# Optimization experiments

Hardware: AMD Instinct MI355X
Metric: run time of the kernel (lower is better)

## Reference

```python
import jax, jax.numpy as jnp
import numpy as np

BN_EPS = 1e-5

def setup_inputs() -> dict:
    key = jax.random.key(0)
    ks = jax.random.split(key, 7)
    B, D, A = 16384, 768, 51
    s = 1.0 / np.sqrt(D)
    return {
        "x": jax.random.normal(ks[0], (B, D), dtype=jnp.float32),
        "W_embed": jax.random.uniform(ks[1], (D, D), minval=-s, maxval=s, dtype=jnp.float32),
        "b_embed": jax.random.uniform(ks[2], (D,), minval=-s, maxval=s, dtype=jnp.float32),
        "W_attr": jax.random.uniform(ks[3], (A, D), minval=-s, maxval=s, dtype=jnp.float32),  # stacked per-attribute (dim->1) heads
        "b_attr": jax.random.uniform(ks[4], (A,), minval=-s, maxval=s, dtype=jnp.float32),
        "gamma": jnp.ones((A,), dtype=jnp.float32),
        "beta": jnp.zeros((A,), dtype=jnp.float32),
    }

def reference(x, W_embed, b_embed, W_attr, b_attr, gamma, beta):
    # word_embed: Linear(dim, dim)
    h = x @ W_embed.T + b_embed                      # [B, D]
    # fused per-attribute heads: cat of attr_num (dim->1) linears == one (dim->attr_num) matmul
    logits = h @ W_attr.T + b_attr                    # [B, A]
    # BatchNorm1d (training mode: batch statistics, biased variance)
    mean = jnp.mean(logits, axis=0)
    var = jnp.var(logits, axis=0)
    y = (logits - mean) * jax.lax.rsqrt(var + BN_EPS) * gamma + beta
    return y
```

## Files before the change

kernel.cpp:

```cpp
#include <hip/hip_runtime.h>
#include <hip/hip_bf16.h>

typedef _Float16 halfx8 __attribute__((ext_vector_type(8)));
typedef _Float16 halfx4 __attribute__((ext_vector_type(4)));
typedef float floatx4 __attribute__((ext_vector_type(4)));

#define GLOBAL_AS __attribute__((address_space(1)))
#define LDS_AS __attribute__((address_space(3)))

__device__ __forceinline__ void async_copy_16(const _Float16* g, _Float16* l) {
    __builtin_amdgcn_global_load_lds((GLOBAL_AS void*)g, (LDS_AS void*)l, 16, 0, 0);
}

#define PM 16384
#define PD 768
#define PA 51
#define PA_PAD 64


__global__ void convert_w_kernel(const float* __restrict__ We, const float* __restrict__ Wa,
                                 _Float16* __restrict__ we16, _Float16* __restrict__ wa16,
                                 float* __restrict__ stats) {
    int b = blockIdx.x, t = threadIdx.x;
    if (b < 576) {
        int idx = b * 256 + t;
        float4 v = ((const float4*)We)[idx];
        halfx4 h;
        h[0] = (_Float16)v.x; h[1] = (_Float16)v.y; h[2] = (_Float16)v.z; h[3] = (_Float16)v.w;
        *(halfx4*)(we16 + (size_t)idx * 4) = h;
    } else if (b < 624) {
        int j = (b - 576) * 256 + t;
        halfx4 h;
        if (j < (PA * PD) / 4) {
            float4 v = ((const float4*)Wa)[j];
            h[0] = (_Float16)v.x; h[1] = (_Float16)v.y; h[2] = (_Float16)v.z; h[3] = (_Float16)v.w;
        } else {
            h[0] = (_Float16)0.f; h[1] = (_Float16)0.f; h[2] = (_Float16)0.f; h[3] = (_Float16)0.f;
        }
        *(halfx4*)(wa16 + (size_t)j * 4) = h;
    } else {
        if (t < 128) stats[t] = 0.f;
    }
}

__global__ __launch_bounds__(256, 3) void gemm1_kernel(
    const float* __restrict__ X,
    const _Float16* __restrict__ B,
    const float* __restrict__ bias,
    _Float16* __restrict__ H)
{
    __shared__ _Float16 As[128 * 64];
    __shared__ _Float16 Bs[128 * 64];
    const int tid = threadIdx.x;
    const int wave = tid >> 6;
    const int lane = tid & 63;
    const int quad = lane >> 4;
    const int l16 = lane & 15;
    const int wm = wave >> 1;
    const int wn = wave & 1;

    int b = blockIdx.x;
    int xcd = b & 7;
    int q = b >> 3;
    int mt = xcd * 16 + (q & 15);
    int nt = q >> 4;
    const int row0 = mt * 128;
    const int col0 = nt * 128;

    const int r_in = lane >> 3;
    const int csw = (lane & 7) ^ r_in;
    const int ksw = csw * 8;

    const float* Ag = X + (size_t)row0 * PD + ksw;
    const _Float16* Bg = B + (size_t)col0 * PD + ksw;

    floatx4 acc[4][4];
    #pragma unroll
    for (int i = 0; i < 4; ++i)
        #pragma unroll
        for (int j = 0; j < 4; ++j)
            acc[i][j] = (floatx4){0.f, 0.f, 0.f, 0.f};

    for (int kt = 0; kt < PD; kt += 64) {
        #pragma unroll
        for (int j = 0; j < 4; ++j) {
            int i = wave * 4 + j;
            const float* ap = Ag + (size_t)(i * 8 + r_in) * PD + kt;
            float4 v0 = *(const float4*)(ap);
            float4 v1 = *(const float4*)(ap + 4);
            halfx8 h;
            h[0] = (_Float16)v0.x; h[1] = (_Float16)v0.y;
            h[2] = (_Float16)v0.z; h[3] = (_Float16)v0.w;
            h[4] = (_Float16)v1.x; h[5] = (_Float16)v1.y;
            h[6] = (_Float16)v1.z; h[7] = (_Float16)v1.w;
            *(halfx8*)&As[(i * 8 + r_in) * 64 + (lane & 7) * 8] = h;
            async_copy_16(Bg + (size_t)(i * 8 + r_in) * PD + kt, &Bs[i * 512]);
        }
        __syncthreads();
        #pragma unroll
        for (int ks = 0; ks < 2; ++ks) {
            halfx8 af[4], bf[4];
            #pragma unroll
            for (int mi = 0; mi < 4; ++mi)
                af[mi] = *(const halfx8*)&As[(wm * 64 + mi * 16 + l16) * 64 +
                                             (((ks * 4 + quad) ^ (l16 & 7)) << 3)];
            #pragma unroll
            for (int ni = 0; ni < 4; ++ni)
                bf[ni] = *(const halfx8*)&Bs[(wn * 64 + ni * 16 + l16) * 64 +
                                             (((ks * 4 + quad) ^ (l16 & 7)) << 3)];
            #pragma unroll
            for (int mi = 0; mi < 4; ++mi)
                #pragma unroll
                for (int ni = 0; ni < 4; ++ni)
                    acc[mi][ni] = __builtin_amdgcn_mfma_f32_16x16x32_f16(af[mi], bf[ni], acc[mi][ni], 0, 0, 0);
        }
        __syncthreads();
    }

    #pragma unroll
    for (int ni = 0; ni < 4; ++ni) {
        int col = col0 + wn * 64 + ni * 16 + l16;
        float bv = bias[col];
        #pragma unroll
        for (int mi = 0; mi < 4; ++mi) {
            int rowb = row0 + wm * 64 + mi * 16 + quad * 4;
            #pragma unroll
            for (int r = 0; r < 4; ++r)
                H[(size_t)(rowb + r) * PD + col] = (_Float16)(acc[mi][ni][r] + bv);
        }
    }
}

__global__ __launch_bounds__(256) void gemm2_kernel(
    const _Float16* __restrict__ Hm,
    const _Float16* __restrict__ Wa,
    const float* __restrict__ b_attr,
    float* __restrict__ logits,
    float* __restrict__ stats)
{
    __shared__ _Float16 As[64 * 64];
    __shared__ _Float16 Bs[64 * 64];
    __shared__ float s_sum[64];
    __shared__ float s_ssq[64];
    const int tid = threadIdx.x;
    const int wave = tid >> 6;
    const int lane = tid & 63;
    const int quad = lane >> 4;
    const int l16 = lane & 15;
    const int row0 = blockIdx.x * 64;
    const int r_in = lane >> 3;
    const int ksw = ((lane & 7) ^ r_in) * 8;

    if (tid < 64) { s_sum[tid] = 0.f; s_ssq[tid] = 0.f; }

    const _Float16* Ag = Hm + (size_t)row0 * PD + ksw;
    const _Float16* Bg = Wa + ksw;

    floatx4 acc[4];
    #pragma unroll
    for (int j = 0; j < 4; ++j)
        acc[j] = (floatx4){0.f, 0.f, 0.f, 0.f};

    for (int kt = 0; kt < PD; kt += 64) {
        #pragma unroll
        for (int j = 0; j < 2; ++j) {
            int i = wave * 2 + j;
            async_copy_16(Ag + (size_t)(i * 8 + r_in) * PD + kt, &As[i * 512]);
            async_copy_16(Bg + (size_t)(i * 8 + r_in) * PD + kt, &Bs[i * 512]);
        }
        __syncthreads();
        #pragma unroll
        for (int ks = 0; ks < 2; ++ks) {
            halfx8 af, bf[4];
            af = *(const halfx8*)&As[(wave * 16 + l16) * 64 +
                                     (((ks * 4 + quad) ^ (l16 & 7)) << 3)];
            #pragma unroll
            for (int ni = 0; ni < 4; ++ni)
                bf[ni] = *(const halfx8*)&Bs[(ni * 16 + l16) * 64 +
                                             (((ks * 4 + quad) ^ (l16 & 7)) << 3)];
            #pragma unroll
            for (int ni = 0; ni < 4; ++ni)
                acc[ni] = __builtin_amdgcn_mfma_f32_16x16x32_f16(af, bf[ni], acc[ni], 0, 0, 0);
        }
        __syncthreads();
    }

    #pragma unroll
    for (int ni = 0; ni < 4; ++ni) {
        int col = ni * 16 + l16;
        if (col < PA) {
            float bv = b_attr[col];
            float ps = 0.f, pss = 0.f;
            int rowb = row0 + wave * 16 + quad * 4;
            #pragma unroll
            for (int r = 0; r < 4; ++r) {
                float v = acc[ni][r] + bv;
                logits[(size_t)(rowb + r) * PA + col] = v;
                ps += v; pss += v * v;
            }
            atomicAdd(&s_sum[col], ps);
            atomicAdd(&s_ssq[col], pss);
        }
    }
    __syncthreads();
    if (tid < PA) {
        atomicAdd(&stats[tid], s_sum[tid]);
        atomicAdd(&stats[64 + tid], s_ssq[tid]);
    }
}

__global__ void bn_finalize_kernel(const float* __restrict__ logits,
                                   const float* __restrict__ stats,
                                   const float* __restrict__ gamma,
                                   const float* __restrict__ beta,
                                   float* __restrict__ out, int total) {
    __shared__ float s_scale[PA];
    __shared__ float s_shift[PA];
    int t = threadIdx.x;
    if (t < PA) {
        const float invB = 1.0f / (float)PM;
        float mean = stats[t] * invB;
        float var = stats[64 + t] * invB - mean * mean;
        float inv = rsqrtf(var + 1e-5f);
        float g = gamma[t] * inv;
        s_scale[t] = g;
        s_shift[t] = beta[t] - mean * g;
    }
    __syncthreads();
    int idx = blockIdx.x * 256 + t;
    if (idx < total) {
        int col = idx % PA;
        out[idx] = logits[idx] * s_scale[col] + s_shift[col];
    }
}

extern "C" void kernel_launch(void* const* d_in, const int* in_sizes, int n_in,
                              void* d_out, int out_size, void* d_ws, size_t ws_size,
                              hipStream_t stream) {
    const float* x       = (const float*)d_in[0];
    const float* W_embed = (const float*)d_in[1];
    const float* b_embed = (const float*)d_in[2];
    const float* W_attr  = (const float*)d_in[3];
    const float* b_attr  = (const float*)d_in[4];
    const float* gamma   = (const float*)d_in[5];
    const float* beta    = (const float*)d_in[6];
    float* out = (float*)d_out;

    char* ws = (char*)d_ws;
    _Float16* we16   = (_Float16*)(ws);
    _Float16* wa16   = (_Float16*)(ws + 1179648);
    _Float16* h_f16  = (_Float16*)(ws + 1277952);
    float*    logits = (float*)   (ws + 26443776);
    float*    stats  = (float*)   (ws + 29786112);

    convert_w_kernel<<<625, 256, 0, stream>>>(W_embed, W_attr, we16, wa16, stats);
    gemm1_kernel<<<768, 256, 0, stream>>>(x, we16, b_embed, h_f16);
    gemm2_kernel<<<256, 256, 0, stream>>>(h_f16, wa16, b_attr, logits, stats);
    bn_finalize_kernel<<<3264, 256, 0, stream>>>(logits, stats, gamma, beta, out, PM * PA);
}
```

Measured before the change: 155.2 us.

## Fold the two linear layers into one combined weight before the skinny GEMM

Precomputes Wc = W_attr·W_embed (51x768) and a combined bias in a small kernel, so the large 16384x768x768 GEMM and the fp16 H intermediate go away. The remaining kernel streams x directly into LDS as fp32 with async copies and converts it to fp16 at fragment load, then multiplies by the folded weight. This removes most of the FLOPs and the H round-trip through memory. In exchange it adds a serial precompute of about 30M FMAs on 53 blocks and changes rounding order, since Wc is formed in fp32 and then cast to fp16.

```diff
diff --git a/kernel.cpp b/kernel.cpp
--- a/kernel.cpp
+++ b/kernel.cpp
@@ -8,172 +8,114 @@
 #define GLOBAL_AS __attribute__((address_space(1)))
 #define LDS_AS __attribute__((address_space(3)))
 
-__device__ __forceinline__ void async_copy_16(const _Float16* g, _Float16* l) {
+__device__ __forceinline__ void async_copy_16(const void* g, void* l) {
     __builtin_amdgcn_global_load_lds((GLOBAL_AS void*)g, (LDS_AS void*)l, 16, 0, 0);
 }
 
 #define PM 16384
 #define PD 768
 #define PA 51
-#define PA_PAD 64
-
-
-__global__ void convert_w_kernel(const float* __restrict__ We, const float* __restrict__ Wa,
-                                 _Float16* __restrict__ we16, _Float16* __restrict__ wa16,
-                                 float* __restrict__ stats) {
+
+
+__global__ __launch_bounds__(192) void precompute_kernel(
+    const float* __restrict__ We, const float* __restrict__ Wa,
+    const float* __restrict__ b_embed, const float* __restrict__ b_attr,
+    _Float16* __restrict__ wc16, float* __restrict__ bc, float* __restrict__ stats)
+{
     int b = blockIdx.x, t = threadIdx.x;
-    if (b < 576) {
-        int idx = b * 256 + t;
-        float4 v = ((const float4*)We)[idx];
+    if (b < PA) {
+        int d0 = t * 4;
+        const float* war = Wa + (size_t)b * PD;
+        float a0 = 0.f, a1 = 0.f, a2 = 0.f, a3 = 0.f;
+        #pragma unroll 8
+        for (int k = 0; k < PD; ++k) {
+            float w = war[k];
+            floatx4 v = *(const floatx4*)(We + (size_t)k * PD + d0);
+            a0 += w * v[0]; a1 += w * v[1]; a2 += w * v[2]; a3 += w * v[3];
+        }
         halfx4 h;
-        h[0] = (_Float16)v.x; h[1] = (_Float16)v.y; h[2] = (_Float16)v.z; h[3] = (_Float16)v.w;
-        *(halfx4*)(we16 + (size_t)idx * 4) = h;
-    } else if (b < 624) {
-        int j = (b - 576) * 256 + t;
-        halfx4 h;
-        if (j < (PA * PD) / 4) {
-            float4 v = ((const float4*)Wa)[j];
-            h[0] = (_Float16)v.x; h[1] = (_Float16)v.y; h[2] = (_Float16)v.z; h[3] = (_Float16)v.w;
-        } else {
-            h[0] = (_Float16)0.f; h[1] = (_Float16)0.f; h[2] = (_Float16)0.f; h[3] = (_Float16)0.f;
-        }
-        *(halfx4*)(wa16 + (size_t)j * 4) = h;
+        h[0] = (_Float16)a0; h[1] = (_Float16)a1; h[2] = (_Float16)a2; h[3] = (_Float16)a3;
+        *(halfx4*)(wc16 + (size_t)b * PD + d0) = h;
+    } else if (b == PA) {
+        halfx8 z;
+        #pragma unroll
+        for (int j = 0; j < 8; ++j) z[j] = (_Float16)0.f;
+        for (int i = t; i < 1248; i += 192)
+            *(halfx8*)(wc16 + PA * PD + i * 8) = z;
+        if (t < 128) stats[t] = 0.f;
     } else {
-        if (t < 128) stats[t] = 0.f;
-    }
-}
-
-__global__ __launch_bounds__(256, 3) void gemm1_kernel(
+        if (t < PA) {
+            const float* war = Wa + (size_t)t * PD;
+            float acc = 0.f;
+            #pragma unroll 4
+            for (int k = 0; k < PD; k += 4) {
+                floatx4 w = *(const floatx4*)(war + k);
+                floatx4 e = *(const floatx4*)(b_embed + k);
+                acc += w[0] * e[0] + w[1] * e[1] + w[2] * e[2] + w[3] * e[3];
+            }
+            bc[t] = acc + b_attr[t];
+        }
+    }
+}
+
+__global__ __launch_bounds__(256) void skinny_gemm_kernel(
     const float* __restrict__ X,
-    const _Float16* __restrict__ B,
-    const float* __restrict__ bias,
-    _Float16* __restrict__ H)
-{
-    __shared__ _Float16 As[128 * 64];
-    __shared__ _Float16 Bs[128 * 64];
-    const int tid = threadIdx.x;
-    const int wave = tid >> 6;
-    const int lane = tid & 63;
-    const int quad = lane >> 4;
-    const int l16 = lane & 15;
-    const int wm = wave >> 1;
-    const int wn = wave & 1;
-
-    int b = blockIdx.x;
-    int xcd = b & 7;
-    int q = b >> 3;
-    int mt = xcd * 16 + (q & 15);
-    int nt = q >> 4;
-    const int row0 = mt * 128;
-    const int col0 = nt * 128;
-
-    const int r_in = lane >> 3;
-    const int csw = (lane & 7) ^ r_in;
-    const int ksw = csw * 8;
-
-    const float* Ag = X + (size_t)row0 * PD + ksw;
-    const _Float16* Bg = B + (size_t)col0 * PD + ksw;
-
-    floatx4 acc[4][4];
-    #pragma unroll
-    for (int i = 0; i < 4; ++i)
-        #pragma unroll
-        for (int j = 0; j < 4; ++j)
-            acc[i][j] = (floatx4){0.f, 0.f, 0.f, 0.f};
-
-    for (int kt = 0; kt < PD; kt += 64) {
-        #pragma unroll
-        for (int j = 0; j < 4; ++j) {
-            int i = wave * 4 + j;
-            const float* ap = Ag + (size_t)(i * 8 + r_in) * PD + kt;
-            float4 v0 = *(const float4*)(ap);
-            float4 v1 = *(const float4*)(ap + 4);
-            halfx8 h;
-            h[0] = (_Float16)v0.x; h[1] = (_Float16)v0.y;
-            h[2] = (_Float16)v0.z; h[3] = (_Float16)v0.w;
-            h[4] = (_Float16)v1.x; h[5] = (_Float16)v1.y;
-            h[6] = (_Float16)v1.z; h[7] = (_Float16)v1.w;
-            *(halfx8*)&As[(i * 8 + r_in) * 64 + (lane & 7) * 8] = h;
-            async_copy_16(Bg + (size_t)(i * 8 + r_in) * PD + kt, &Bs[i * 512]);
-        }
-        __syncthreads();
-        #pragma unroll
-        for (int ks = 0; ks < 2; ++ks) {
-            halfx8 af[4], bf[4];
-            #pragma unroll
-            for (int mi = 0; mi < 4; ++mi)
-                af[mi] = *(const halfx8*)&As[(wm * 64 + mi * 16 + l16) * 64 +
-                                             (((ks * 4 + quad) ^ (l16 & 7)) << 3)];
-            #pragma unroll
-            for (int ni = 0; ni < 4; ++ni)
-                bf[ni] = *(const halfx8*)&Bs[(wn * 64 + ni * 16 + l16) * 64 +
-                                             (((ks * 4 + quad) ^ (l16 & 7)) << 3)];
-            #pragma unroll
-            for (int mi = 0; mi < 4; ++mi)
-                #pragma unroll
-                for (int ni = 0; ni < 4; ++ni)
-                    acc[mi][ni] = __builtin_amdgcn_mfma_f32_16x16x32_f16(af[mi], bf[ni], acc[mi][ni], 0, 0, 0);
-        }
-        __syncthreads();
-    }
-
-    #pragma unroll
-    for (int ni = 0; ni < 4; ++ni) {
-        int col = col0 + wn * 64 + ni * 16 + l16;
-        float bv = bias[col];
-        #pragma unroll
-        for (int mi = 0; mi < 4; ++mi) {
-            int rowb = row0 + wm * 64 + mi * 16 + quad * 4;
-            #pragma unroll
-            for (int r = 0; r < 4; ++r)
-                H[(size_t)(rowb + r) * PD + col] = (_Float16)(acc[mi][ni][r] + bv);
-        }
-    }
-}
-
-__global__ __launch_bounds__(256) void gemm2_kernel(
-    const _Float16* __restrict__ Hm,
-    const _Float16* __restrict__ Wa,
-    const float* __restrict__ b_attr,
+    const _Float16* __restrict__ Wc,
+    const float* __restrict__ bc,
     float* __restrict__ logits,
     float* __restrict__ stats)
 {
-    __shared__ _Float16 As[64 * 64];
+    __shared__ float As[64 * 64];
     __shared__ _Float16 Bs[64 * 64];
     __shared__ float s_sum[64];
     __shared__ float s_ssq[64];
+
     const int tid = threadIdx.x;
     const int wave = tid >> 6;
     const int lane = tid & 63;
     const int quad = lane >> 4;
     const int l16 = lane & 15;
     const int row0 = blockIdx.x * 64;
-    const int r_in = lane >> 3;
-    const int ksw = ((lane & 7) ^ r_in) * 8;
 
     if (tid < 64) { s_sum[tid] = 0.f; s_ssq[tid] = 0.f; }
 
-    const _Float16* Ag = Hm + (size_t)row0 * PD + ksw;
-    const _Float16* Bg = Wa + ksw;
+    const int a_r  = lane >> 4;
+    const int a_sl = lane & 15;
+    const int b_r  = lane >> 3;
+    const int b_sl = lane & 7;
 
     floatx4 acc[4];
     #pragma unroll
-    for (int j = 0; j < 4; ++j)
-        acc[j] = (floatx4){0.f, 0.f, 0.f, 0.f};
+    for (int j = 0; j < 4; ++j) acc[j] = (floatx4){0.f, 0.f, 0.f, 0.f};
 
     for (int kt = 0; kt < PD; kt += 64) {
         #pragma unroll
+        for (int j = 0; j < 4; ++j) {
+            int g = wave * 4 + j;
+            int r = g * 4 + a_r;
+            int c = a_sl ^ (r & 7);
+            async_copy_16(X + (size_t)(row0 + r) * PD + kt + c * 4, &As[g * 256]);
+        }
+        #pragma unroll
         for (int j = 0; j < 2; ++j) {
-            int i = wave * 2 + j;
-            async_copy_16(Ag + (size_t)(i * 8 + r_in) * PD + kt, &As[i * 512]);
-            async_copy_16(Bg + (size_t)(i * 8 + r_in) * PD + kt, &Bs[i * 512]);
+            int g = wave * 2 + j;
+            int r = g * 8 + b_r;
+            int c = b_sl ^ (r & 7);
+            async_copy_16(Wc + (size_t)r * PD + kt + c * 8, &Bs[g * 512]);
         }
         __syncthreads();
         #pragma unroll
         for (int ks = 0; ks < 2; ++ks) {
-            halfx8 af, bf[4];
-            af = *(const halfx8*)&As[(wave * 16 + l16) * 64 +
-                                     (((ks * 4 + quad) ^ (l16 & 7)) << 3)];
+            int r = wave * 16 + l16;
+            int c0 = ks * 8 + quad * 2;
+            floatx4 p0 = *(const floatx4*)&As[r * 64 + ((c0 ^ (l16 & 7)) << 2)];
+            floatx4 p1 = *(const floatx4*)&As[r * 64 + (((c0 + 1) ^ (l16 & 7)) << 2)];
+            halfx8 af;
+            af[0] = (_Float16)p0[0]; af[1] = (_Float16)p0[1];
+            af[2] = (_Float16)p0[2]; af[3] = (_Float16)p0[3];
+            af[4] = (_Float16)p1[0]; af[5] = (_Float16)p1[1];
+            af[6] = (_Float16)p1[2]; af[7] = (_Float16)p1[3];
+            halfx8 bf[4];
             #pragma unroll
             for (int ni = 0; ni < 4; ++ni)
                 bf[ni] = *(const halfx8*)&Bs[(ni * 16 + l16) * 64 +
@@ -189,7 +131,7 @@
     for (int ni = 0; ni < 4; ++ni) {
         int col = ni * 16 + l16;
         if (col < PA) {
-            float bv = b_attr[col];
+            float bv = bc[col];
             float ps = 0.f, pss = 0.f;
             int rowb = row0 + wave * 16 + quad * 4;
             #pragma unroll
@@ -247,14 +189,12 @@
     float* out = (float*)d_out;
 
     char* ws = (char*)d_ws;
-    _Float16* we16   = (_Float16*)(ws);
-    _Float16* wa16   = (_Float16*)(ws + 1179648);
-    _Float16* h_f16  = (_Float16*)(ws + 1277952);
-    float*    logits = (float*)   (ws + 26443776);
-    float*    stats  = (float*)   (ws + 29786112);
-
-    convert_w_kernel<<<625, 256, 0, stream>>>(W_embed, W_attr, we16, wa16, stats);
-    gemm1_kernel<<<768, 256, 0, stream>>>(x, we16, b_embed, h_f16);
-    gemm2_kernel<<<256, 256, 0, stream>>>(h_f16, wa16, b_attr, logits, stats);
+    _Float16* wc16   = (_Float16*)(ws);
+    float*    bc     = (float*)   (ws + 98304);
+    float*    stats  = (float*)   (ws + 98560);
+    float*    logits = (float*)   (ws + 99072);
+
+    precompute_kernel<<<53, 192, 0, stream>>>(W_embed, W_attr, b_embed, b_attr, wc16, bc, stats);
+    skinny_gemm_kernel<<<256, 256, 0, stream>>>(x, wc16, bc, logits, stats);
     bn_finalize_kernel<<<3264, 256, 0, stream>>>(logits, stats, gamma, beta, out, PM * PA);
 }
```

New measurement: 152.2 us. Within noise of the previous version (-2.0%).
